# Performance work log

Measured on AMD Instinct MI355X. Metric: run time of the kernel, lower is better.

Reference implementation:

```python
import jax, jax.numpy as jnp
import numpy as np

B, H, W, C = 2, 256, 256, 180
WS, OWS, NH = 8, 12, 6  # window, overlap window, heads
RPB_N = (WS + OWS - 1) ** 2  # 361


def _ln(x, w, b):
    mu = x.mean(-1, keepdims=True)
    var = ((x - mu) ** 2).mean(-1, keepdims=True)
    return (x - mu) / jnp.sqrt(var + 1e-5) * w + b


def _dwt2(x):  # (b,h,w,c) -> (b,h/2,w/2,4c) haar, order [LL,LH,HL,HH]
    a = x[:, 0::2, 0::2]
    bb = x[:, 0::2, 1::2]
    cc = x[:, 1::2, 0::2]
    dd = x[:, 1::2, 1::2]
    ll = (a + bb + cc + dd) * 0.5
    lh = (-a - bb + cc + dd) * 0.5
    hl = (-a + bb - cc + dd) * 0.5
    hh = (a - bb - cc + dd) * 0.5
    return jnp.concatenate([ll, lh, hl, hh], axis=-1)


def _idwt2(y):  # (b,h2,w2,4c) -> (b,2h2,2w2,c)
    ll, lh, hl, hh = jnp.split(y, 4, axis=-1)
    a = (ll - lh - hl + hh) * 0.5
    bb = (ll - lh + hl - hh) * 0.5
    cc = (ll + lh - hl - hh) * 0.5
    dd = (ll + lh + hl + hh) * 0.5
    b_, h2, w2, c = a.shape
    even = jnp.stack([a, bb], axis=3).reshape(b_, h2, 2 * w2, c)
    odd = jnp.stack([cc, dd], axis=3).reshape(b_, h2, 2 * w2, c)
    return jnp.stack([even, odd], axis=2).reshape(b_, 2 * h2, 2 * w2, c)


def _win_part(x, ws):  # (b,h,w,c) -> (b*nw, ws, ws, c)
    b, h, w, c = x.shape
    x = x.reshape(b, h // ws, ws, w // ws, ws, c)
    return x.transpose(0, 1, 3, 2, 4, 5).reshape(-1, ws, ws, c)


def _win_rev(win, ws, h, w):  # inverse of _win_part
    b = win.shape[0] // ((h // ws) * (w // ws))
    x = win.reshape(b, h // ws, w // ws, ws, ws, -1)
    return x.transpose(0, 1, 3, 2, 4, 5).reshape(b, h, w, -1)


def _unfold_windows(x, ws, ows):  # nn.Unfold(kernel=ows, stride=ws, pad=ows-ws)
    b, hs, wss, c = x.shape
    pad = ows - ws
    xp = jnp.pad(x, ((0, 0), (pad, pad), (pad, pad), (0, 0)))
    nwh = hs // ws
    idx = (jnp.arange(nwh) * ws)[:, None] + jnp.arange(ows)[None, :]  # (nwh, ows)
    p = xp[:, idx][:, :, :, idx]  # (b, nwh, ows, nwh, ows, c)
    p = p.transpose(0, 1, 3, 2, 4, 5)  # (b, ih, iw, kh, kw, c)
    return p.reshape(b * nwh * nwh, ows * ows, c)


def _forward(x, cross_x, rpi, h, w, norm1_w, norm1_b, normc_w, normc_b,
             q_w, q_b, k_w, k_b, v_w, v_b, rpb, proj_w, proj_b,
             norm2_w, norm2_b, fc1_w, fc1_b, fc2_w, fc2_b):
    b, _, c = x.shape
    shortcut = x
    xn = _ln(x, norm1_w, norm1_b).reshape(b, h, w, c)
    _ = _ln(cross_x, normc_w, normc_b)  # computed in original wav branch, unused
    xd = _dwt2(xn)  # (b, h/2, w/2, 4c)
    q = xd @ q_w + q_b  # (b, h/2, w/2, c)
    k = xd @ k_w + k_b  # (b, h/2, w/2, c)
    v = xd @ v_w + v_b  # (b, h/2, w/2, 4c)
    scale = (c // NH) ** -0.5
    qw = _win_part(q, WS).reshape(-1, WS * WS, c)
    kw = _unfold_windows(k, WS, OWS)
    vw = _unfold_windows(v, WS, OWS)
    b_, nq = qw.shape[0], WS * WS
    n, d = OWS * OWS, c // NH
    qh = qw.reshape(b_, nq, NH, d).transpose(0, 2, 1, 3) * scale
    kh = kw.reshape(b_, n, NH, d).transpose(0, 2, 1, 3)
    vh = vw.reshape(b_, n, NH, 4 * d).transpose(0, 2, 1, 3)
    bias = rpb[rpi.reshape(-1)].reshape(nq, n, NH).transpose(2, 0, 1)  # (NH,nq,n)
    attn = jax.nn.softmax(jnp.einsum('bhqd,bhkd->bhqk', qh, kh) + bias[None], axis=-1)
    o = jnp.einsum('bhqk,bhkd->bhqd', attn, vh).transpose(0, 2, 1, 3).reshape(b_, nq, 4 * c)
    o = o.reshape(-1, WS, WS, 4 * c)
    xw = _win_rev(o, WS, h // 2, w // 2)  # (b, h/2, w/2, 4c)
    xr = _idwt2(xw).reshape(b, h * w, c)
    x1 = xr @ proj_w + proj_b + shortcut
    y = _ln(x1, norm2_w, norm2_b)
    y = jax.nn.gelu(y @ fc1_w + fc1_b, approximate=False) @ fc2_w + fc2_b
    return x1 + y


def setup_inputs() -> dict:
    key = jax.random.key(0)
    ks = jax.random.split(key, 12)
    nrm = lambda k, s: (jax.random.normal(k, s, jnp.float32) * 0.02)
    return {
        'x': jax.random.normal(ks[0], (B, H * W, C), jnp.float32),
        'cross_x': jax.random.normal(ks[1], (B, H * W, C), jnp.float32),
        'rpi': jax.random.randint(ks[2], (WS * WS, OWS * OWS), 0, RPB_N),
        'h': H, 'w': W,
        'norm1_w': jnp.ones((C,), jnp.float32), 'norm1_b': jnp.zeros((C,), jnp.float32),
        'normc_w': jnp.ones((C,), jnp.float32), 'normc_b': jnp.zeros((C,), jnp.float32),
        'q_w': nrm(ks[3], (4 * C, C)), 'q_b': jnp.zeros((C,), jnp.float32),
        'k_w': nrm(ks[4], (4 * C, C)), 'k_b': jnp.zeros((C,), jnp.float32),
        'v_w': nrm(ks[5], (4 * C, 4 * C)), 'v_b': jnp.zeros((4 * C,), jnp.float32),
        'rpb': nrm(ks[6], (RPB_N, NH)),
        'proj_w': nrm(ks[7], (C, C)), 'proj_b': jnp.zeros((C,), jnp.float32),
        'norm2_w': jnp.ones((C,), jnp.float32), 'norm2_b': jnp.zeros((C,), jnp.float32),
        'fc1_w': nrm(ks[8], (C, 2 * C)), 'fc1_b': jnp.zeros((2 * C,), jnp.float32),
        'fc2_w': nrm(ks[9], (2 * C, C)), 'fc2_b': jnp.zeros((C,), jnp.float32),
    }


def reference(x, cross_x, rpi, h, w, norm1_w, norm1_b, normc_w, normc_b,
              q_w, q_b, k_w, k_b, v_w, v_b, rpb, proj_w, proj_b,
              norm2_w, norm2_b, fc1_w, fc1_b, fc2_w, fc2_b):
    return _forward(x, cross_x, rpi, h, w, norm1_w, norm1_b, normc_w, normc_b,
                    q_w, q_b, k_w, k_b, v_w, v_b, rpb, proj_w, proj_b,
                    norm2_w, norm2_b, fc1_w, fc1_b, fc2_w, fc2_b)
```

## Files before the change

### kernel.cpp

```cpp
#include <hip/hip_runtime.h>
#include <hip/hip_bf16.h>
#include <stdint.h>

using bf16 = __hip_bfloat16;
typedef __attribute__((ext_vector_type(8))) short bf16x8;
typedef __attribute__((ext_vector_type(4))) float f32x4;

union U8 { uint4 u; bf16x8 h; };

static __device__ __forceinline__ float b2f(bf16 v) { return __bfloat162float(v); }
static __device__ __forceinline__ bf16  f2b(float v) { return __float2bfloat16(v); }
static __device__ __forceinline__ float toF(float v) { return v; }
static __device__ __forceinline__ float toF(bf16 v)  { return __bfloat162float(v); }
static __device__ __forceinline__ void stF(float* p, float v) { *p = v; }
static __device__ __forceinline__ void stF(bf16* p,  float v) { *p = f2b(v); }
static __device__ __forceinline__ float bfu(unsigned short x) {
  union { unsigned int i; float f; } z; z.i = ((unsigned int)x) << 16; return z.f;
}

static __device__ __forceinline__ void gload16(const bf16* g, const short* l) {
  __builtin_amdgcn_global_load_lds(
      (const __attribute__((address_space(1))) void*)g,
      (__attribute__((address_space(3))) void*)l, 16, 0, 0);
}

__global__ __launch_bounds__(256) void convert_wt_kernel(
    const float* __restrict__ w, bf16* __restrict__ wt, int K, int N, int Kp)
{
  int idx = blockIdx.x * 256 + threadIdx.x;
  if (idx >= N * Kp) return;
  int n = idx / Kp, k = idx % Kp;
  float v = (k < K) ? w[(size_t)k * N + n] : 0.f;
  wt[idx] = f2b(v);
}

__global__ __launch_bounds__(256) void concat_bias_kernel(
    const float* __restrict__ qb, const float* __restrict__ kb,
    const float* __restrict__ vb, float* __restrict__ o)
{
  int i = blockIdx.x * 256 + threadIdx.x;
  if (i >= 1080) return;
  o[i] = (i < 180) ? qb[i] : (i < 360) ? kb[i - 180] : vb[i - 360];
}

__global__ __launch_bounds__(256) void bias_pre_kernel(
    const int* __restrict__ rpi, const float* __restrict__ rpb, float* __restrict__ bias_f)
{
  int e = blockIdx.x * 256 + threadIdx.x;
  if (e >= 6 * 64 * 144) return;
  int hh = e / 9216, rk = e % 9216;
  bias_f[e] = rpb[rpi[rk] * 6 + hh];
}

__global__ __launch_bounds__(256) void ln_dwt_kernel(
    const float* __restrict__ x, const float* __restrict__ w, const float* __restrict__ bia,
    bf16* __restrict__ xd)
{
  __shared__ float nrm[4][180];
  int blk = blockIdx.x;
  int j = blk & 127; int i = (blk >> 7) & 127; int b = blk >> 14;
  int wave = threadIdx.x >> 6, lane = threadIdx.x & 63;
  int ty = wave >> 1, tx = wave & 1;
  size_t tok = (size_t)b * 65536 + (size_t)(2 * i + ty) * 256 + (size_t)(2 * j + tx);
  const float* xp = x + tok * 180;
  float v0 = xp[lane];
  float v1 = xp[lane + 64];
  float v2 = (lane < 52) ? xp[lane + 128] : 0.f;
  float s = v0 + v1 + v2, ss = v0 * v0 + v1 * v1 + v2 * v2;
  #pragma unroll
  for (int m = 32; m; m >>= 1) { s += __shfl_xor(s, m); ss += __shfl_xor(ss, m); }
  float mu = s * (1.f / 180.f);
  float rstd = rsqrtf(ss * (1.f / 180.f) - mu * mu + 1e-5f);
  nrm[wave][lane]      = (v0 - mu) * rstd * w[lane]      + bia[lane];
  nrm[wave][lane + 64] = (v1 - mu) * rstd * w[lane + 64] + bia[lane + 64];
  if (lane < 52)
    nrm[wave][lane + 128] = (v2 - mu) * rstd * w[lane + 128] + bia[lane + 128];
  __syncthreads();
  bf16* op = xd + (size_t)blk * 720;
  for (int o = threadIdx.x; o < 720; o += 256) {
    int g = o / 180, c = o % 180;
    float a = nrm[0][c], bb = nrm[1][c], cc = nrm[2][c], dd = nrm[3][c];
    float r = (g == 0) ? (a + bb + cc + dd)
            : (g == 1) ? (-a - bb + cc + dd)
            : (g == 2) ? (-a + bb - cc + dd)
                       : (a - bb - cc + dd);
    op[o] = f2b(r * 0.5f);
  }
}

__global__ __launch_bounds__(256) void ln_kernel(
    const bf16* __restrict__ x, const float* __restrict__ w, const float* __restrict__ bia,
    bf16* __restrict__ y)
{
  int wave = threadIdx.x >> 6, lane = threadIdx.x & 63;
  size_t tok = (size_t)blockIdx.x * 4 + wave;
  const bf16* xp = x + tok * 180;
  float v0 = b2f(xp[lane]);
  float v1 = b2f(xp[lane + 64]);
  float v2 = (lane < 52) ? b2f(xp[lane + 128]) : 0.f;
  float s = v0 + v1 + v2, ss = v0 * v0 + v1 * v1 + v2 * v2;
  #pragma unroll
  for (int m = 32; m; m >>= 1) { s += __shfl_xor(s, m); ss += __shfl_xor(ss, m); }
  float mu = s * (1.f / 180.f);
  float rstd = rsqrtf(ss * (1.f / 180.f) - mu * mu + 1e-5f);
  bf16* yp = y + tok * 192;
  yp[lane]      = f2b((v0 - mu) * rstd * w[lane]      + bia[lane]);
  yp[lane + 64] = f2b((v1 - mu) * rstd * w[lane + 64] + bia[lane + 64]);
  if (lane < 52)
    yp[lane + 128] = f2b((v2 - mu) * rstd * w[lane + 128] + bia[lane + 128]);
  else
    yp[lane + 128] = f2b(0.f);
}

template <int EP, typename TRes, typename TOut>
__global__ __launch_bounds__(256) void gemm_mfma(
    const bf16* __restrict__ A, const bf16* __restrict__ Wt,
    const float* __restrict__ bias, const TRes* __restrict__ res,
    TOut* __restrict__ out, int N, int lda, int Kp, int ldout, int ldres)
{
  __shared__ __align__(16) short Al[128 * 32];
  __shared__ __align__(16) short Bl[192 * 32];
  int tid = threadIdx.x;
  int wave = tid >> 6, lane = tid & 63;
  int wy = wave >> 1, wx = wave & 1;
  int m0 = blockIdx.x * 128, n0 = blockIdx.y * 192;

  f32x4 acc[4][6] = {};

  int ar0 = tid >> 2;
  int ac  = (tid & 3) * 8;
  const bf16* gA0 = A + (size_t)(m0 + ar0) * lda + ac;
  const bf16* gA1 = A + (size_t)(m0 + 64 + ar0) * lda + ac;
  int br0 = n0 + ar0, br1 = n0 + ar0 + 64, br2 = n0 + ar0 + 128;
  br0 = (br0 < N) ? br0 : (N - 1);
  br1 = (br1 < N) ? br1 : (N - 1);
  br2 = (br2 < N) ? br2 : (N - 1);
  const bf16* gB0 = Wt + (size_t)br0 * Kp + ac;
  const bf16* gB1 = Wt + (size_t)br1 * Kp + ac;
  const bf16* gB2 = Wt + (size_t)br2 * Kp + ac;

  int wb = wave * 512;
  int fm = lane & 15, quad = lane >> 4;
  const short* afp = &Al[(wy * 64 + fm) * 32 + quad * 8];
  const short* bfp = &Bl[(wx * 96 + fm) * 32 + quad * 8];

  for (int k0 = 0; k0 < Kp; k0 += 32) {
    __syncthreads();
    gload16(gA0 + k0, &Al[wb]);
    gload16(gA1 + k0, &Al[2048 + wb]);
    gload16(gB0 + k0, &Bl[wb]);
    gload16(gB1 + k0, &Bl[2048 + wb]);
    gload16(gB2 + k0, &Bl[4096 + wb]);
    __syncthreads();

    bf16x8 af0 = *(const bf16x8*)(afp);
    bf16x8 af1 = *(const bf16x8*)(afp + 16 * 32);
    bf16x8 af2 = *(const bf16x8*)(afp + 32 * 32);
    bf16x8 af3 = *(const bf16x8*)(afp + 48 * 32);
    #pragma unroll
    for (int nt = 0; nt < 6; nt++) {
      bf16x8 bfr = *(const bf16x8*)(bfp + nt * 16 * 32);
      acc[0][nt] = __builtin_amdgcn_mfma_f32_16x16x32_bf16(af0, bfr, acc[0][nt], 0, 0, 0);
      acc[1][nt] = __builtin_amdgcn_mfma_f32_16x16x32_bf16(af1, bfr, acc[1][nt], 0, 0, 0);
      acc[2][nt] = __builtin_amdgcn_mfma_f32_16x16x32_bf16(af2, bfr, acc[2][nt], 0, 0, 0);
      acc[3][nt] = __builtin_amdgcn_mfma_f32_16x16x32_bf16(af3, bfr, acc[3][nt], 0, 0, 0);
    }
  }

  #pragma unroll
  for (int nt = 0; nt < 6; nt++) {
    int col = n0 + wx * 96 + nt * 16 + fm;
    if (col >= N) continue;
    float bv = bias[col];
    #pragma unroll
    for (int mt = 0; mt < 4; mt++) {
      int row0 = m0 + wy * 64 + mt * 16 + quad * 4;
      #pragma unroll
      for (int r = 0; r < 4; r++) {
        int row = row0 + r;
        float v = acc[mt][nt][r] + bv;
        if constexpr (EP == 1) v += toF(res[(size_t)row * ldres + col]);
        if constexpr (EP == 2) v = 0.5f * v * (1.f + erff(v * 0.70710678118654752f));
        stF(&out[(size_t)row * ldout + col], v);
      }
    }
  }
}

__global__ __launch_bounds__(256) void attn_kernel(
    const bf16* __restrict__ qkv, const float* __restrict__ bias_f, bf16* __restrict__ xw)
{
  __shared__ short tokl[160];
  __shared__ __align__(16) short Pl[64 * 168];
  __shared__ __align__(16) short Vt[128 * 168];
  const float scale = 0.18257418583505536f;
  int blk = blockIdx.x;
  int hh = blk % 6; int wid = blk / 6;
  int wj = wid & 15; int wi = (wid >> 4) & 15; int b = wid >> 8;
  int tid = threadIdx.x;
  int wave = tid >> 6, lane = tid & 63;
  int fm = lane & 15, quad = lane >> 4;
  const unsigned int* qkvu = (const unsigned int*)qkv;
  int hh15 = hh * 15, hh60 = hh * 60;

  if (tid < 144) {
    int ky = tid / 12, kx = tid % 12;
    int gy = wi * 8 - 4 + ky, gx = wj * 8 - 4 + kx;
    tokl[tid] = (gy >= 0 && gy < 128 && gx >= 0 && gx < 128)
              ? (short)(b * 16384 + gy * 128 + gx) : (short)-1;
  }
  __syncthreads();

  {
    int kg = tid & 15, oct = tid >> 4;
    int colx = (oct & 1) << 4;
    #pragma unroll
    for (int p = 0; p < 10; p++) {
      int kk = p * 16 + kg;
      int t = (kk < 144) ? (int)tokl[kk] : -1;
      U8 vv; vv.u = make_uint4(0, 0, 0, 0);
      if (oct < 15 && t >= 0)
        vv.u = *(const uint4*)(qkvu + (size_t)t * 540 + 180 + hh60 + oct * 4);
      short* wp = &Vt[oct * 8 * 168 + (kk ^ colx)];
      #pragma unroll
      for (int jj = 0; jj < 8; jj++) wp[jj * 168] = vv.h[jj];
    }
  }

  f32x4 sacc[9] = {};
  {
    U8 qf;
    int r = wave * 16 + fm;
    int gy = wi * 8 + (r >> 3), gx = wj * 8 + (r & 7);
    const unsigned int* qp = qkvu + (size_t)(b * 16384 + gy * 128 + gx) * 540 + hh15 + quad * 4;
    qf.u.x = qp[0]; qf.u.y = qp[1]; qf.u.z = qp[2]; qf.u.w = qp[3];
    if (quad == 3) qf.u.w = 0;
    #pragma unroll
    for (int nt = 0; nt < 9; nt++) {
      int t = (int)tokl[nt * 16 + fm];
      U8 kf; kf.u = make_uint4(0, 0, 0, 0);
      if (t >= 0) {
        const unsigned int* kp = qkvu + (size_t)t * 540 + 90 + hh15 + quad * 4;
        kf.u.x = kp[0]; kf.u.y = kp[1]; kf.u.z = kp[2]; kf.u.w = kp[3];
      }
      if (quad == 3) kf.u.w = 0;
      sacc[nt] = __builtin_amdgcn_mfma_f32_16x16x32_bf16(qf.h, kf.h, sacc[nt], 0, 0, 0);
    }
  }

  float sv[9][4];
  const float* bias_g = bias_f + hh * 9216;
  {
    #pragma unroll
    for (int r = 0; r < 4; r++) {
      int row = wave * 16 + quad * 4 + r;
      #pragma unroll
      for (int nt = 0; nt < 9; nt++)
        sv[nt][r] = sacc[nt][r] * scale + bias_g[row * 144 + nt * 16 + fm];
    }
    float mr[4], sr[4];
    #pragma unroll
    for (int r = 0; r < 4; r++) {
      float m = sv[0][r];
      #pragma unroll
      for (int nt = 1; nt < 9; nt++) m = fmaxf(m, sv[nt][r]);
      #pragma unroll
      for (int sh = 1; sh < 16; sh <<= 1) m = fmaxf(m, __shfl_xor(m, sh));
      mr[r] = m;
    }
    #pragma unroll
    for (int r = 0; r < 4; r++) {
      float s = 0.f;
      #pragma unroll
      for (int nt = 0; nt < 9; nt++) { sv[nt][r] = __expf(sv[nt][r] - mr[r]); s += sv[nt][r]; }
      #pragma unroll
      for (int sh = 1; sh < 16; sh <<= 1) s += __shfl_xor(s, sh);
      sr[r] = 1.f / s;
    }
    #pragma unroll
    for (int r = 0; r < 4; r++)
      #pragma unroll
      for (int nt = 0; nt < 9; nt++) sv[nt][r] *= sr[r];
  }

  #pragma unroll
  for (int r = 0; r < 4; r++) {
    int row = wave * 16 + quad * 4 + r;
    #pragma unroll
    for (int nt = 0; nt < 9; nt++)
      Pl[row * 168 + nt * 16 + fm] = (short)__bfloat16_as_ushort(f2b(sv[nt][r]));
  }
  #pragma unroll
  for (int j2 = 0; j2 < 2; j2++) {
    int idx = lane * 2 + j2;
    int row = wave * 16 + (idx >> 3);
    *(unsigned int*)&Pl[row * 168 + 144 + (idx & 7) * 2] = 0u;
  }
  __syncthreads();

  int sread = (fm & 8) << 1;
  bf16x8 pf[5];
  const short* prow = &Pl[(wave * 16 + fm) * 168];
  #pragma unroll
  for (int ks = 0; ks < 5; ks++) pf[ks] = *(const bf16x8*)&prow[ks * 32 + quad * 8];
  f32x4 oacc[8] = {};
  #pragma unroll
  for (int ks = 0; ks < 5; ks++) {
    #pragma unroll
    for (int nt = 0; nt < 8; nt++) {
      bf16x8 vf = *(const bf16x8*)&Vt[(nt * 16 + fm) * 168 + ((ks * 32 + quad * 8) ^ sread)];
      oacc[nt] = __builtin_amdgcn_mfma_f32_16x16x32_bf16(pf[ks], vf, oacc[nt], 0, 0, 0);
    }
  }
  #pragma unroll
  for (int nt = 0; nt < 8; nt++) {
    int col = nt * 16 + fm;
    if (col >= 120) continue;
    #pragma unroll
    for (int r = 0; r < 4; r++) {
      int row = wave * 16 + quad * 4 + r;
      int gy = wi * 8 + (row >> 3), gx = wj * 8 + (row & 7);
      xw[((size_t)b * 16384 + (size_t)gy * 128 + gx) * 720 + hh * 120 + col] = f2b(oacc[nt][r]);
    }
  }
}

__global__ __launch_bounds__(256) void idwt_kernel(
    const bf16* __restrict__ xw, bf16* __restrict__ xr)
{
  int gid = blockIdx.x * 256 + threadIdx.x;
  int cu = gid % 24;
  int tokn = gid / 24;
  int c = cu * 8;
  bf16* op = xr + (size_t)tokn * 192 + c;
  uint4 outv = make_uint4(0, 0, 0, 0);
  if (c < 184) {
    int x2 = tokn & 255, y2 = (tokn >> 8) & 255, bb = tokn >> 16;
    int ii = y2 >> 1, jj = x2 >> 1, py = y2 & 1, px = x2 & 1;
    const unsigned short* p = (const unsigned short*)xw
        + ((size_t)bb * 16384 + (size_t)ii * 128 + jj) * 720 + c;
    union QW { uint4 v; uint2 u[2]; unsigned short s[8]; } a_, b_, c_, d_, o_;
    a_.u[0] = *(const uint2*)(p);        a_.u[1] = *(const uint2*)(p + 4);
    b_.u[0] = *(const uint2*)(p + 180);  b_.u[1] = *(const uint2*)(p + 184);
    c_.u[0] = *(const uint2*)(p + 360);  c_.u[1] = *(const uint2*)(p + 364);
    d_.u[0] = *(const uint2*)(p + 540);  d_.u[1] = *(const uint2*)(p + 544);
    #pragma unroll
    for (int t = 0; t < 8; t++) {
      float ll = bfu(a_.s[t]), lh = bfu(b_.s[t]), hl = bfu(c_.s[t]), hv = bfu(d_.s[t]);
      float r;
      if (py == 0) r = (px == 0) ? (ll - lh - hl + hv) : (ll - lh + hl - hv);
      else         r = (px == 0) ? (ll + lh - hl - hv) : (ll + lh + hl + hv);
      o_.s[t] = (c + t < 180) ? __bfloat16_as_ushort(f2b(r * 0.5f)) : (unsigned short)0;
    }
    outv = o_.v;
  }
  *(uint4*)op = outv;
}

extern "C" void kernel_launch(void* const* d_in, const int* in_sizes, int n_in,
                              void* d_out, int out_size, void* d_ws, size_t ws_size,
                              hipStream_t stream) {
  (void)in_sizes; (void)n_in; (void)out_size; (void)ws_size;
  const float* x      = (const float*)d_in[0];
  const int*   rpi    = (const int*)  d_in[2];
  const float* n1w    = (const float*)d_in[5];
  const float* n1b    = (const float*)d_in[6];
  const float* q_w    = (const float*)d_in[9];
  const float* q_b    = (const float*)d_in[10];
  const float* k_w    = (const float*)d_in[11];
  const float* k_b    = (const float*)d_in[12];
  const float* v_w    = (const float*)d_in[13];
  const float* v_b    = (const float*)d_in[14];
  const float* rpb    = (const float*)d_in[15];
  const float* proj_w = (const float*)d_in[16];
  const float* proj_b = (const float*)d_in[17];
  const float* n2w    = (const float*)d_in[18];
  const float* n2b    = (const float*)d_in[19];
  const float* fc1_w  = (const float*)d_in[20];
  const float* fc1_b  = (const float*)d_in[21];
  const float* fc2_w  = (const float*)d_in[22];
  const float* fc2_b  = (const float*)d_in[23];
  float* out = (float*)d_out;

  bf16* xd  = (bf16*)d_ws;
  bf16* qkv = xd + 23592960;
  bf16* x1  = qkv + 35389440;
  bf16* hb  = x1 + 23592960;
  bf16* wts = hb + 47185920;
  bf16* qkvwt = wts;
  bf16* pwt  = qkvwt + 794880;
  bf16* f1wt = pwt + 34560;
  bf16* f2wt = f1wt + 69120;
  float* bias_f = (float*)(f2wt + 69120);
  float* qkv_b  = bias_f + 55296;
  bf16* xw = xd;
  bf16* xr = qkv + 10223616;
  bf16* yb = xd;

  convert_wt_kernel<<<518,  256, 0, stream>>>(q_w,    qkvwt,          720, 180, 736);
  convert_wt_kernel<<<518,  256, 0, stream>>>(k_w,    qkvwt + 132480, 720, 180, 736);
  convert_wt_kernel<<<2071, 256, 0, stream>>>(v_w,    qkvwt + 264960, 720, 720, 736);
  convert_wt_kernel<<<135,  256, 0, stream>>>(proj_w, pwt,  180, 180, 192);
  convert_wt_kernel<<<270,  256, 0, stream>>>(fc1_w,  f1wt, 180, 360, 192);
  convert_wt_kernel<<<270,  256, 0, stream>>>(fc2_w,  f2wt, 360, 180, 384);
  concat_bias_kernel<<<5, 256, 0, stream>>>(q_b, k_b, v_b, qkv_b);
  bias_pre_kernel<<<216, 256, 0, stream>>>(rpi, rpb, bias_f);

  ln_dwt_kernel<<<32768, 256, 0, stream>>>(x, n1w, n1b, xd);
  gemm_mfma<0, float, bf16><<<dim3(256, 6),  256, 0, stream>>>(xd, qkvwt, qkv_b, nullptr, qkv, 1080, 720, 736, 1080, 0);
  attn_kernel<<<3072, 256, 0, stream>>>(qkv, bias_f, xw);
  idwt_kernel<<<12288, 256, 0, stream>>>(xw, xr);
  gemm_mfma<1, float, bf16><<<dim3(1024, 1), 256, 0, stream>>>(xr, pwt, proj_b, x, x1, 180, 192, 192, 180, 180);
  ln_kernel<<<32768, 256, 0, stream>>>(x1, n2w, n2b, yb);
  gemm_mfma<2, float, bf16><<<dim3(1024, 2), 256, 0, stream>>>(yb, f1wt, fc1_b, nullptr, hb, 360, 192, 192, 360, 0);
  gemm_mfma<1, bf16, float><<<dim3(1024, 1), 256, 0, stream>>>(hb, f2wt, fc2_b, x1, out, 180, 360, 384, 180, 180);
}
```

Before: 748.6 us.

## Pipeline GEMM K-loop with 4-stage LDS ring buffer and swizzled layout

Replaces the single-buffered GEMM main loop, which synchronised twice per K step, with a four-buffer LDS ring. Three global-to-LDS stages are kept in flight, gated by vmcnt waits and a single barrier per iteration. The load columns are XOR-swizzled to reduce LDS bank conflicts on fragment reads, and MFMA issue priority is raised. LDS use per block grows about fourfold (roughly 80KB), which lowers occupancy, and the code assumes Kp/32 is at least 3.

```diff
diff --git a/kernel.cpp b/kernel.cpp
--- a/kernel.cpp
+++ b/kernel.cpp
@@ -118,8 +118,8 @@
     const float* __restrict__ bias, const TRes* __restrict__ res,
     TOut* __restrict__ out, int N, int lda, int Kp, int ldout, int ldres)
 {
-  __shared__ __align__(16) short Al[128 * 32];
-  __shared__ __align__(16) short Bl[192 * 32];
+  __shared__ __align__(16) short Al[4][128 * 32];
+  __shared__ __align__(16) short Bl[4][192 * 32];
   int tid = threadIdx.x;
   int wave = tid >> 6, lane = tid & 63;
   int wy = wave >> 1, wx = wave & 1;
@@ -128,48 +128,89 @@
   f32x4 acc[4][6] = {};
 
   int ar0 = tid >> 2;
-  int ac  = (tid & 3) * 8;
-  const bf16* gA0 = A + (size_t)(m0 + ar0) * lda + ac;
-  const bf16* gA1 = A + (size_t)(m0 + 64 + ar0) * lda + ac;
+  int acs = ((tid & 3) ^ ((tid >> 3) & 3)) * 8;
+  const bf16* gA0 = A + (size_t)(m0 + ar0) * lda + acs;
+  const bf16* gA1 = A + (size_t)(m0 + 64 + ar0) * lda + acs;
   int br0 = n0 + ar0, br1 = n0 + ar0 + 64, br2 = n0 + ar0 + 128;
   br0 = (br0 < N) ? br0 : (N - 1);
   br1 = (br1 < N) ? br1 : (N - 1);
   br2 = (br2 < N) ? br2 : (N - 1);
-  const bf16* gB0 = Wt + (size_t)br0 * Kp + ac;
-  const bf16* gB1 = Wt + (size_t)br1 * Kp + ac;
-  const bf16* gB2 = Wt + (size_t)br2 * Kp + ac;
+  const bf16* gB0 = Wt + (size_t)br0 * Kp + acs;
+  const bf16* gB1 = Wt + (size_t)br1 * Kp + acs;
+  const bf16* gB2 = Wt + (size_t)br2 * Kp + acs;
 
   int wb = wave * 512;
   int fm = lane & 15, quad = lane >> 4;
-  const short* afp = &Al[(wy * 64 + fm) * 32 + quad * 8];
-  const short* bfp = &Bl[(wx * 96 + fm) * 32 + quad * 8];
-
-  for (int k0 = 0; k0 < Kp; k0 += 32) {
-    __syncthreads();
-    gload16(gA0 + k0, &Al[wb]);
-    gload16(gA1 + k0, &Al[2048 + wb]);
-    gload16(gB0 + k0, &Bl[wb]);
-    gload16(gB1 + k0, &Bl[2048 + wb]);
-    gload16(gB2 + k0, &Bl[4096 + wb]);
-    __syncthreads();
-
-    bf16x8 af0 = *(const bf16x8*)(afp);
-    bf16x8 af1 = *(const bf16x8*)(afp + 16 * 32);
-    bf16x8 af2 = *(const bf16x8*)(afp + 32 * 32);
-    bf16x8 af3 = *(const bf16x8*)(afp + 48 * 32);
-    #pragma unroll
-    for (int nt = 0; nt < 6; nt++) {
-      bf16x8 bfr = *(const bf16x8*)(bfp + nt * 16 * 32);
-      acc[0][nt] = __builtin_amdgcn_mfma_f32_16x16x32_bf16(af0, bfr, acc[0][nt], 0, 0, 0);
-      acc[1][nt] = __builtin_amdgcn_mfma_f32_16x16x32_bf16(af1, bfr, acc[1][nt], 0, 0, 0);
-      acc[2][nt] = __builtin_amdgcn_mfma_f32_16x16x32_bf16(af2, bfr, acc[2][nt], 0, 0, 0);
-      acc[3][nt] = __builtin_amdgcn_mfma_f32_16x16x32_bf16(af3, bfr, acc[3][nt], 0, 0, 0);
-    }
-  }
-
-  #pragma unroll
-  for (int nt = 0; nt < 6; nt++) {
-    int col = n0 + wx * 96 + nt * 16 + fm;
+  int qsw = (quad ^ ((fm >> 1) & 3)) * 8;
+  const short* afp = &Al[0][(wy * 64 + fm) * 32 + qsw];
+  const short* bfp = &Bl[0][(wx * 96 + fm) * 32 + qsw];
+
+  int nt = Kp >> 5;
+
+  auto stage = [&](int t) {
+    int buf = t & 3, k0 = t * 32;
+    gload16(gA0 + k0, &Al[buf][wb]);
+    gload16(gA1 + k0, &Al[buf][2048 + wb]);
+    gload16(gB0 + k0, &Bl[buf][wb]);
+    gload16(gB1 + k0, &Bl[buf][2048 + wb]);
+    gload16(gB2 + k0, &Bl[buf][4096 + wb]);
+  };
+  auto frag_load = [&](int t, bf16x8 (&af)[4], bf16x8 (&bfr)[6]) {
+    int aoff = (t & 3) * 4096, boff = (t & 3) * 6144;
+    #pragma unroll
+    for (int i = 0; i < 4; i++) af[i] = *(const bf16x8*)(afp + aoff + i * 512);
+    #pragma unroll
+    for (int j = 0; j < 6; j++) bfr[j] = *(const bf16x8*)(bfp + boff + j * 512);
+  };
+  auto mfma_all = [&](bf16x8 (&af)[4], bf16x8 (&bfr)[6]) {
+    __builtin_amdgcn_s_setprio(1);
+    #pragma unroll
+    for (int i = 0; i < 4; i++)
+      #pragma unroll
+      for (int j = 0; j < 6; j++)
+        acc[i][j] = __builtin_amdgcn_mfma_f32_16x16x32_bf16(af[i], bfr[j], acc[i][j], 0, 0, 0);
+    __builtin_amdgcn_s_setprio(0);
+  };
+
+  stage(0); stage(1); stage(2);
+
+  for (int t = 0; t < nt - 3; t++) {
+    asm volatile("s_waitcnt vmcnt(10)" ::: "memory");
+    __builtin_amdgcn_s_barrier();
+    __builtin_amdgcn_sched_barrier(0);
+    bf16x8 af[4], bfr[6];
+    frag_load(t, af, bfr);
+    stage(t + 3);
+    mfma_all(af, bfr);
+  }
+  {
+    asm volatile("s_waitcnt vmcnt(10)" ::: "memory");
+    __builtin_amdgcn_s_barrier();
+    __builtin_amdgcn_sched_barrier(0);
+    bf16x8 af[4], bfr[6];
+    frag_load(nt - 3, af, bfr);
+    mfma_all(af, bfr);
+  }
+  {
+    asm volatile("s_waitcnt vmcnt(5)" ::: "memory");
+    __builtin_amdgcn_s_barrier();
+    __builtin_amdgcn_sched_barrier(0);
+    bf16x8 af[4], bfr[6];
+    frag_load(nt - 2, af, bfr);
+    mfma_all(af, bfr);
+  }
+  {
+    asm volatile("s_waitcnt vmcnt(0)" ::: "memory");
+    __builtin_amdgcn_s_barrier();
+    __builtin_amdgcn_sched_barrier(0);
+    bf16x8 af[4], bfr[6];
+    frag_load(nt - 1, af, bfr);
+    mfma_all(af, bfr);
+  }
+
+  #pragma unroll
+  for (int nt2 = 0; nt2 < 6; nt2++) {
+    int col = n0 + wx * 96 + nt2 * 16 + fm;
     if (col >= N) continue;
     float bv = bias[col];
     #pragma unroll
@@ -178,7 +219,7 @@
       #pragma unroll
       for (int r = 0; r < 4; r++) {
         int row = row0 + r;
-        float v = acc[mt][nt][r] + bv;
+        float v = acc[mt][nt2][r] + bv;
         if constexpr (EP == 1) v += toF(res[(size_t)row * ldres + col]);
         if constexpr (EP == 2) v = 0.5f * v * (1.f + erff(v * 0.70710678118654752f));
         stF(&out[(size_t)row * ldout + col], v);
```

After: 727.6 us. 2.8% less time.

## Load GEMM MFMA fragments directly from global memory instead of staging through LDS

Applied to the files above, without the earlier changes.

The GEMM kernel no longer stages A and B tiles in shared memory with global_load_lds and two barriers per k-step. Each wave now loads its own MFMA operand fragments straight from global memory into registers. This removes the barriers and the LDS traffic, but each A row is reloaded by both wx waves and each B row by both wy waves. Those duplicate reads depend on the caches, and the loads are no longer cooperatively coalesced.

```diff
diff --git a/kernel.cpp b/kernel.cpp
--- a/kernel.cpp
+++ b/kernel.cpp
@@ -16,12 +16,6 @@
 static __device__ __forceinline__ void stF(bf16* p,  float v) { *p = f2b(v); }
 static __device__ __forceinline__ float bfu(unsigned short x) {
   union { unsigned int i; float f; } z; z.i = ((unsigned int)x) << 16; return z.f;
-}
-
-static __device__ __forceinline__ void gload16(const bf16* g, const short* l) {
-  __builtin_amdgcn_global_load_lds(
-      (const __attribute__((address_space(1))) void*)g,
-      (__attribute__((address_space(3))) void*)l, 16, 0, 0);
 }
 
 __global__ __launch_bounds__(256) void convert_wt_kernel(
@@ -118,58 +112,47 @@
     const float* __restrict__ bias, const TRes* __restrict__ res,
     TOut* __restrict__ out, int N, int lda, int Kp, int ldout, int ldres)
 {
-  __shared__ __align__(16) short Al[128 * 32];
-  __shared__ __align__(16) short Bl[192 * 32];
   int tid = threadIdx.x;
   int wave = tid >> 6, lane = tid & 63;
   int wy = wave >> 1, wx = wave & 1;
   int m0 = blockIdx.x * 128, n0 = blockIdx.y * 192;
+  int fm = lane & 15, quad = lane >> 4;
 
   f32x4 acc[4][6] = {};
 
-  int ar0 = tid >> 2;
-  int ac  = (tid & 3) * 8;
-  const bf16* gA0 = A + (size_t)(m0 + ar0) * lda + ac;
-  const bf16* gA1 = A + (size_t)(m0 + 64 + ar0) * lda + ac;
-  int br0 = n0 + ar0, br1 = n0 + ar0 + 64, br2 = n0 + ar0 + 128;
-  br0 = (br0 < N) ? br0 : (N - 1);
-  br1 = (br1 < N) ? br1 : (N - 1);
-  br2 = (br2 < N) ? br2 : (N - 1);
-  const bf16* gB0 = Wt + (size_t)br0 * Kp + ac;
-  const bf16* gB1 = Wt + (size_t)br1 * Kp + ac;
-  const bf16* gB2 = Wt + (size_t)br2 * Kp + ac;
-
-  int wb = wave * 512;
-  int fm = lane & 15, quad = lane >> 4;
-  const short* afp = &Al[(wy * 64 + fm) * 32 + quad * 8];
-  const short* bfp = &Bl[(wx * 96 + fm) * 32 + quad * 8];
+  const bf16* pa0 = A + (size_t)(m0 + wy * 64 +  0 + fm) * lda + quad * 8;
+  const bf16* pa1 = A + (size_t)(m0 + wy * 64 + 16 + fm) * lda + quad * 8;
+  const bf16* pa2 = A + (size_t)(m0 + wy * 64 + 32 + fm) * lda + quad * 8;
+  const bf16* pa3 = A + (size_t)(m0 + wy * 64 + 48 + fm) * lda + quad * 8;
+  const bf16* pb[6];
+  #pragma unroll
+  for (int j = 0; j < 6; j++) {
+    int br = n0 + wx * 96 + j * 16 + fm;
+    br = (br < N) ? br : (N - 1);
+    pb[j] = Wt + (size_t)br * Kp + quad * 8;
+  }
 
   for (int k0 = 0; k0 < Kp; k0 += 32) {
-    __syncthreads();
-    gload16(gA0 + k0, &Al[wb]);
-    gload16(gA1 + k0, &Al[2048 + wb]);
-    gload16(gB0 + k0, &Bl[wb]);
-    gload16(gB1 + k0, &Bl[2048 + wb]);
-    gload16(gB2 + k0, &Bl[4096 + wb]);
-    __syncthreads();
-
-    bf16x8 af0 = *(const bf16x8*)(afp);
-    bf16x8 af1 = *(const bf16x8*)(afp + 16 * 32);
-    bf16x8 af2 = *(const bf16x8*)(afp + 32 * 32);
-    bf16x8 af3 = *(const bf16x8*)(afp + 48 * 32);
-    #pragma unroll
-    for (int nt = 0; nt < 6; nt++) {
-      bf16x8 bfr = *(const bf16x8*)(bfp + nt * 16 * 32);
-      acc[0][nt] = __builtin_amdgcn_mfma_f32_16x16x32_bf16(af0, bfr, acc[0][nt], 0, 0, 0);
-      acc[1][nt] = __builtin_amdgcn_mfma_f32_16x16x32_bf16(af1, bfr, acc[1][nt], 0, 0, 0);
-      acc[2][nt] = __builtin_amdgcn_mfma_f32_16x16x32_bf16(af2, bfr, acc[2][nt], 0, 0, 0);
-      acc[3][nt] = __builtin_amdgcn_mfma_f32_16x16x32_bf16(af3, bfr, acc[3][nt], 0, 0, 0);
-    }
-  }
-
-  #pragma unroll
-  for (int nt = 0; nt < 6; nt++) {
-    int col = n0 + wx * 96 + nt * 16 + fm;
+    U8 a0, a1, a2, a3, b[6];
+    a0.u = *(const uint4*)(pa0 + k0);
+    a1.u = *(const uint4*)(pa1 + k0);
+    a2.u = *(const uint4*)(pa2 + k0);
+    a3.u = *(const uint4*)(pa3 + k0);
+    #pragma unroll
+    for (int j = 0; j < 6; j++) b[j].u = *(const uint4*)(pb[j] + k0);
+
+    #pragma unroll
+    for (int j = 0; j < 6; j++) {
+      acc[0][j] = __builtin_amdgcn_mfma_f32_16x16x32_bf16(a0.h, b[j].h, acc[0][j], 0, 0, 0);
+      acc[1][j] = __builtin_amdgcn_mfma_f32_16x16x32_bf16(a1.h, b[j].h, acc[1][j], 0, 0, 0);
+      acc[2][j] = __builtin_amdgcn_mfma_f32_16x16x32_bf16(a2.h, b[j].h, acc[2][j], 0, 0, 0);
+      acc[3][j] = __builtin_amdgcn_mfma_f32_16x16x32_bf16(a3.h, b[j].h, acc[3][j], 0, 0, 0);
+    }
+  }
+
+  #pragma unroll
+  for (int nt2 = 0; nt2 < 6; nt2++) {
+    int col = n0 + wx * 96 + nt2 * 16 + fm;
     if (col >= N) continue;
     float bv = bias[col];
     #pragma unroll
@@ -178,7 +161,7 @@
       #pragma unroll
       for (int r = 0; r < 4; r++) {
         int row = row0 + r;
-        float v = acc[mt][nt][r] + bv;
+        float v = acc[mt][nt2][r] + bv;
         if constexpr (EP == 1) v += toF(res[(size_t)row * ldres + col]);
         if constexpr (EP == 2) v = 0.5f * v * (1.f + erff(v * 0.70710678118654752f));
         stF(&out[(size_t)row * ldout + col], v);
```

Result: slower. 796.6 us (+6.4%).
